# Performance work log

Hardware: AMD Instinct MI355X
Metric: run time of the kernel (lower is better)

## Reference

```python
import jax, jax.numpy as jnp
import numpy as np


def setup_inputs() -> dict:
    key = jax.random.key(0)
    k1, k2 = jax.random.split(key)
    x = jax.random.normal(k1, (16, 256, 128, 128), dtype=jnp.float32)
    # Conv2d(2, 1, 7, padding=3, bias=False) weight, OIHW layout
    conv_w = jax.random.normal(k2, (1, 2, 7, 7), dtype=jnp.float32) * 0.1
    return {"x": x, "conv_w": conv_w}


def reference(x, conv_w):
    # channel-wise mean and max pooling -> [B, 1, H, W] each
    avg_pool = jnp.mean(x, axis=1, keepdims=True)
    max_pool = jnp.max(x, axis=1, keepdims=True)
    cat = jnp.concatenate([avg_pool, max_pool], axis=1)  # [B, 2, H, W]
    # 7x7 conv, SAME padding (pad=3), NCHW / OIHW
    out = jax.lax.conv_general_dilated(
        cat, conv_w,
        window_strides=(1, 1),
        padding=((3, 3), (3, 3)),
        dimension_numbers=("NCHW", "OIHW", "NCHW"),
    )  # [B, 1, H, W]
    M = jax.nn.sigmoid(out)
    return x * M
```

## Files before the change

### kernel.cpp

```cpp
#include <hip/hip_runtime.h>
#include <math.h>

#define BB 16
#define CC 256
#define HH 128
#define WW 128
#define HWSZ (HH * WW)

__global__ __launch_bounds__(256) void pool_kernel(const float* __restrict__ x,
                                                   float* __restrict__ avg_out,
                                                   float* __restrict__ max_out) {
    const int tf4   = threadIdx.x & 31;
    const int split = threadIdx.x >> 5;
    const int g0    = blockIdx.x * 32;
    const int p0    = g0 * 4;
    const int b     = p0 / HWSZ;
    const int hwb   = p0 % HWSZ;
    const int hw    = hwb + tf4 * 4;

    const float* xb = x + (size_t)b * CC * HWSZ + hw;

    float4 s = make_float4(0.f, 0.f, 0.f, 0.f);
    float4 m = make_float4(-INFINITY, -INFINITY, -INFINITY, -INFINITY);

    const int c0 = split * 32;
    #pragma unroll 8
    for (int i = 0; i < 32; ++i) {
        float4 v = *(const float4*)(xb + (size_t)(c0 + i) * HWSZ);
        s.x += v.x; s.y += v.y; s.z += v.z; s.w += v.w;
        m.x = fmaxf(m.x, v.x); m.y = fmaxf(m.y, v.y);
        m.z = fmaxf(m.z, v.z); m.w = fmaxf(m.w, v.w);
    }

    __shared__ float4 sS[8][32];
    __shared__ float4 sM[8][32];
    sS[split][tf4] = s;
    sM[split][tf4] = m;
    __syncthreads();

    for (int off = 4; off >= 1; off >>= 1) {
        if (split < off) {
            float4 a  = sS[split][tf4], bb2 = sS[split + off][tf4];
            a.x += bb2.x; a.y += bb2.y; a.z += bb2.z; a.w += bb2.w;
            sS[split][tf4] = a;
            float4 ma = sM[split][tf4], mb = sM[split + off][tf4];
            ma.x = fmaxf(ma.x, mb.x); ma.y = fmaxf(ma.y, mb.y);
            ma.z = fmaxf(ma.z, mb.z); ma.w = fmaxf(ma.w, mb.w);
            sM[split][tf4] = ma;
        }
        __syncthreads();
    }

    if (split == 0) {
        float4 a = sS[0][tf4];
        const float inv = 1.0f / CC;
        a.x *= inv; a.y *= inv; a.z *= inv; a.w *= inv;
        *(float4*)(avg_out + (size_t)b * HWSZ + hw) = a;
        *(float4*)(max_out + (size_t)b * HWSZ + hw) = sM[0][tf4];
    }
}

__global__ __launch_bounds__(256) void conv_kernel(const float* __restrict__ avg_in,
                                                   const float* __restrict__ max_in,
                                                   const float* __restrict__ wgt,
                                                   float* __restrict__ Mout) {
    __shared__ float sw[98];
    if (threadIdx.x < 98) sw[threadIdx.x] = wgt[threadIdx.x];
    __syncthreads();

    const int idx = blockIdx.x * blockDim.x + threadIdx.x;
    const int b  = idx / HWSZ;
    const int hw = idx % HWSZ;
    const int h  = hw >> 7;
    const int w  = hw & 127;

    const float* ap = avg_in + (size_t)b * HWSZ;
    const float* mp = max_in + (size_t)b * HWSZ;

    float acc = 0.f;
    #pragma unroll
    for (int kh = 0; kh < 7; ++kh) {
        const int hh = h + kh - 3;
        if (hh < 0 || hh >= HH) continue;
        #pragma unroll
        for (int kw = 0; kw < 7; ++kw) {
            const int ww2 = w + kw - 3;
            if (ww2 < 0 || ww2 >= WW) continue;
            const int off = hh * WW + ww2;
            acc += ap[off] * sw[kh * 7 + kw];
            acc += mp[off] * sw[49 + kh * 7 + kw];
        }
    }
    Mout[idx] = 1.0f / (1.0f + expf(-acc));
}

__global__ __launch_bounds__(256) void mul_kernel(const float* __restrict__ x,
                                                  const float* __restrict__ Mv,
                                                  float* __restrict__ out) {
    const int n4 = BB * CC * HWSZ / 4;
    const int stride = gridDim.x * blockDim.x;
    for (int i = blockIdx.x * blockDim.x + threadIdx.x; i < n4; i += stride) {
        const int b   = i >> 20;
        const int hw4 = i & 4095;
        float4 xv = ((const float4*)x)[i];
        float4 mv = *(const float4*)(Mv + (size_t)b * HWSZ + hw4 * 4);
        float4 o;
        o.x = xv.x * mv.x; o.y = xv.y * mv.y;
        o.z = xv.z * mv.z; o.w = xv.w * mv.w;
        ((float4*)out)[i] = o;
    }
}

extern "C" void kernel_launch(void* const* d_in, const int* in_sizes, int n_in,
                              void* d_out, int out_size, void* d_ws, size_t ws_size,
                              hipStream_t stream) {
    const float* x   = (const float*)d_in[0];
    const float* wgt = (const float*)d_in[1];
    float* out = (float*)d_out;

    float* avg_p = (float*)d_ws;
    float* max_p = avg_p + (size_t)BB * HWSZ;
    float* Mbuf  = max_p + (size_t)BB * HWSZ;

    pool_kernel<<<2048, 256, 0, stream>>>(x, avg_p, max_p);

    conv_kernel<<<(BB * HWSZ) / 256, 256, 0, stream>>>(avg_p, max_p, wgt, Mbuf);

    mul_kernel<<<4096, 256, 0, stream>>>(x, Mbuf, out);
}
```

Baseline: 172.7 us.

## Fuse conv+sigmoid into multiply kernel and widen pooling blocks

Merges the conv/sigmoid kernel with the broadcast multiply: each block computes the attention map for a two-row strip into shared memory, then streams all 256 channels of x for that strip using nontemporal loads and stores. This drops the intermediate M buffer round trip and one kernel launch. The pooling kernel is also reshaped to 64 float4 columns with 4 channel splits of 64 channels each, which halves the block count and shortens the reduction. The fused kernel has only 1024 blocks, each doing a lot of streaming work, so occupancy and load balance may change.

```diff
diff --git a/kernel.cpp b/kernel.cpp
--- a/kernel.cpp
+++ b/kernel.cpp
@@ -7,41 +7,41 @@
 #define WW 128
 #define HWSZ (HH * WW)
 
+typedef float floatx4 __attribute__((ext_vector_type(4)));
+
 __global__ __launch_bounds__(256) void pool_kernel(const float* __restrict__ x,
                                                    float* __restrict__ avg_out,
                                                    float* __restrict__ max_out) {
-    const int tf4   = threadIdx.x & 31;
-    const int split = threadIdx.x >> 5;
-    const int g0    = blockIdx.x * 32;
-    const int p0    = g0 * 4;
-    const int b     = p0 / HWSZ;
-    const int hwb   = p0 % HWSZ;
-    const int hw    = hwb + tf4 * 4;
+    const int tf4   = threadIdx.x & 63;
+    const int split = threadIdx.x >> 6;
+    const int p0    = blockIdx.x * 256;
+    const int b     = p0 >> 14;
+    const int hw    = (p0 & (HWSZ - 1)) + tf4 * 4;
 
     const float* xb = x + (size_t)b * CC * HWSZ + hw;
 
     float4 s = make_float4(0.f, 0.f, 0.f, 0.f);
     float4 m = make_float4(-INFINITY, -INFINITY, -INFINITY, -INFINITY);
 
-    const int c0 = split * 32;
+    const int c0 = split * 64;
     #pragma unroll 8
-    for (int i = 0; i < 32; ++i) {
+    for (int i = 0; i < 64; ++i) {
         float4 v = *(const float4*)(xb + (size_t)(c0 + i) * HWSZ);
         s.x += v.x; s.y += v.y; s.z += v.z; s.w += v.w;
         m.x = fmaxf(m.x, v.x); m.y = fmaxf(m.y, v.y);
         m.z = fmaxf(m.z, v.z); m.w = fmaxf(m.w, v.w);
     }
 
-    __shared__ float4 sS[8][32];
-    __shared__ float4 sM[8][32];
+    __shared__ float4 sS[4][64];
+    __shared__ float4 sM[4][64];
     sS[split][tf4] = s;
     sM[split][tf4] = m;
     __syncthreads();
 
-    for (int off = 4; off >= 1; off >>= 1) {
+    for (int off = 2; off >= 1; off >>= 1) {
         if (split < off) {
-            float4 a  = sS[split][tf4], bb2 = sS[split + off][tf4];
-            a.x += bb2.x; a.y += bb2.y; a.z += bb2.z; a.w += bb2.w;
+            float4 a  = sS[split][tf4], b2 = sS[split + off][tf4];
+            a.x += b2.x; a.y += b2.y; a.z += b2.z; a.w += b2.w;
             sS[split][tf4] = a;
             float4 ma = sM[split][tf4], mb = sM[split + off][tf4];
             ma.x = fmaxf(ma.x, mb.x); ma.y = fmaxf(ma.y, mb.y);
@@ -60,54 +60,60 @@
     }
 }
 
-__global__ __launch_bounds__(256) void conv_kernel(const float* __restrict__ avg_in,
-                                                   const float* __restrict__ max_in,
-                                                   const float* __restrict__ wgt,
-                                                   float* __restrict__ Mout) {
+__global__ __launch_bounds__(256) void convmul_kernel(const float* __restrict__ x,
+                                                      const float* __restrict__ avg_p,
+                                                      const float* __restrict__ max_p,
+                                                      const float* __restrict__ wgt,
+                                                      float* __restrict__ out) {
     __shared__ float sw[98];
-    if (threadIdx.x < 98) sw[threadIdx.x] = wgt[threadIdx.x];
+    __shared__ float sMl[256];
+
+    const int tid = threadIdx.x;
+    if (tid < 98) sw[tid] = wgt[tid];
     __syncthreads();
 
-    const int idx = blockIdx.x * blockDim.x + threadIdx.x;
-    const int b  = idx / HWSZ;
-    const int hw = idx % HWSZ;
-    const int h  = hw >> 7;
-    const int w  = hw & 127;
+    const int strip = blockIdx.x;
+    const int b     = strip >> 6;
+    const int h0    = (strip & 63) * 2;
 
-    const float* ap = avg_in + (size_t)b * HWSZ;
-    const float* mp = max_in + (size_t)b * HWSZ;
+    {
+        const int hl = tid >> 7;
+        const int w  = tid & 127;
+        const int h  = h0 + hl;
+        const float* ap = avg_p + (size_t)b * HWSZ;
+        const float* mp = max_p + (size_t)b * HWSZ;
 
-    float acc = 0.f;
-    #pragma unroll
-    for (int kh = 0; kh < 7; ++kh) {
-        const int hh = h + kh - 3;
-        if (hh < 0 || hh >= HH) continue;
+        float acc = 0.f;
         #pragma unroll
-        for (int kw = 0; kw < 7; ++kw) {
-            const int ww2 = w + kw - 3;
-            if (ww2 < 0 || ww2 >= WW) continue;
-            const int off = hh * WW + ww2;
-            acc += ap[off] * sw[kh * 7 + kw];
-            acc += mp[off] * sw[49 + kh * 7 + kw];
+        for (int kh = 0; kh < 7; ++kh) {
+            const int hh = h + kh - 3;
+            if (hh < 0 || hh >= HH) continue;
+            #pragma unroll
+            for (int kw = 0; kw < 7; ++kw) {
+                const int ww2 = w + kw - 3;
+                if (ww2 < 0 || ww2 >= WW) continue;
+                const int off = hh * WW + ww2;
+                acc += ap[off] * sw[kh * 7 + kw];
+                acc += mp[off] * sw[49 + kh * 7 + kw];
+            }
         }
+        sMl[tid] = 1.0f / (1.0f + expf(-acc));
     }
-    Mout[idx] = 1.0f / (1.0f + expf(-acc));
-}
+    __syncthreads();
 
-__global__ __launch_bounds__(256) void mul_kernel(const float* __restrict__ x,
-                                                  const float* __restrict__ Mv,
-                                                  float* __restrict__ out) {
-    const int n4 = BB * CC * HWSZ / 4;
-    const int stride = gridDim.x * blockDim.x;
-    for (int i = blockIdx.x * blockDim.x + threadIdx.x; i < n4; i += stride) {
-        const int b   = i >> 20;
-        const int hw4 = i & 4095;
-        float4 xv = ((const float4*)x)[i];
-        float4 mv = *(const float4*)(Mv + (size_t)b * HWSZ + hw4 * 4);
-        float4 o;
-        o.x = xv.x * mv.x; o.y = xv.y * mv.y;
-        o.z = xv.z * mv.z; o.w = xv.w * mv.w;
-        ((float4*)out)[i] = o;
+    const int g    = tid & 63;
+    const int csub = tid >> 6;
+    const floatx4 mv = ((const floatx4*)sMl)[g];
+
+    const size_t base = (size_t)b * CC * HWSZ + (size_t)h0 * WW + (size_t)g * 4;
+    const float* xp = x + base;
+    float*       op = out + base;
+
+    #pragma unroll 4
+    for (int c = 0; c < 64; ++c) {
+        const size_t coff = (size_t)(c * 4 + csub) * HWSZ;
+        floatx4 xv = __builtin_nontemporal_load((const floatx4*)(xp + coff));
+        __builtin_nontemporal_store(xv * mv, (floatx4*)(op + coff));
     }
 }
 
@@ -120,11 +126,8 @@
 
     float* avg_p = (float*)d_ws;
     float* max_p = avg_p + (size_t)BB * HWSZ;
-    float* Mbuf  = max_p + (size_t)BB * HWSZ;
 
-    pool_kernel<<<2048, 256, 0, stream>>>(x, avg_p, max_p);
+    pool_kernel<<<1024, 256, 0, stream>>>(x, avg_p, max_p);
 
-    conv_kernel<<<(BB * HWSZ) / 256, 256, 0, stream>>>(avg_p, max_p, wgt, Mbuf);
-
-    mul_kernel<<<4096, 256, 0, stream>>>(x, Mbuf, out);
+    convmul_kernel<<<1024, 256, 0, stream>>>(x, avg_p, max_p, wgt, out);
 }
```

Result: faster. 145.1 us (-16.0%).
